# Performance work log

Hardware: AMD Instinct MI355X
Metric: run time of the kernel (lower is better)

Reference implementation:

```python
import jax, jax.numpy as jnp
import numpy as np

M = 8
EPS = 1e-5


def _bn(x, gamma, beta):
    # x: [T, N, C]; torch BatchNorm1d on [T, C, N] (training mode) normalizes
    # over batch and length dims -> axes (0, 1) here, biased variance.
    mean = jnp.mean(x, axis=(0, 1))
    var = jnp.var(x, axis=(0, 1))
    return (x - mean) * jax.lax.rsqrt(var + EPS) * gamma + beta


def setup_inputs() -> dict:
    key = jax.random.key(0)
    T, N, E = 128, 256, 128
    ks = jax.random.split(key, 16)
    s = 1.0 / np.sqrt(E)
    inp = {
        "node": jax.random.normal(ks[0], (T, N, E), dtype=jnp.float32),
        "Wq": jax.random.uniform(ks[1], (E, E), jnp.float32, -s, s),
        "bq": jax.random.uniform(ks[2], (E,), jnp.float32, -s, s),
        "Wk": jax.random.uniform(ks[3], (E, E), jnp.float32, -s, s),
        "bk": jax.random.uniform(ks[4], (E,), jnp.float32, -s, s),
        "Wv": jax.random.uniform(ks[5], (E, E), jnp.float32, -s, s),
        "bv": jax.random.uniform(ks[6], (E,), jnp.float32, -s, s),
        "Ww": jax.random.uniform(ks[7], (E, E), jnp.float32, -s, s),
        "bw": jax.random.uniform(ks[8], (E,), jnp.float32, -s, s),
        "Wf1": jax.random.uniform(ks[9], (4 * E, E), jnp.float32, -s, s),
        "bf1": jax.random.uniform(ks[10], (4 * E,), jnp.float32, -s, s),
        "Wf2": jax.random.uniform(ks[11], (E, 4 * E), jnp.float32, -0.5 * s, 0.5 * s),
        "bf2": jax.random.uniform(ks[12], (E,), jnp.float32, -0.5 * s, 0.5 * s),
        "g1": jnp.ones((E,), jnp.float32),
        "be1": jnp.zeros((E,), jnp.float32),
        "g2": jnp.ones((E,), jnp.float32),
        "be2": jnp.zeros((E,), jnp.float32),
        "temp_len": T,
    }
    return inp


def reference(node, Wq, bq, Wk, bk, Wv, bv, Ww, bw, Wf1, bf1, Wf2, bf2,
              g1, be1, g2, be2, temp_len):
    T, N, E = node.shape
    D = E // M          # head dim = 16
    dk = E / M          # softmax scale denominator (embedding_size / M)

    q = (node @ Wq.T + bq).reshape(T, N, M, D)
    k = (node @ Wk.T + bk).reshape(T, N, M, D)
    v = (node @ Wv.T + bv).reshape(T, N, M, D)

    # scores[t,n,j,m] = sum_d q[t,n,m,d]*k[t,j,m,d] / sqrt(dk)
    scores = jnp.einsum('tnmd,tjmd->tnjm', q, k) / jnp.sqrt(jnp.float32(dk))
    attn = jax.nn.softmax(scores, axis=2)  # softmax over key dim (dim=2)

    # out[t,n,m,d] = sum_j attn[t,n,j,m] * v[t,j,m,d]
    out = jnp.einsum('tnjm,tjmd->tnmd', attn, v).reshape(T, N, E)

    x = out @ Ww.T + bw + node
    x = _bn(x, g1, be1)

    x1 = jax.nn.relu(x @ Wf1.T + bf1) @ Wf2.T + bf2
    x = x + x1
    x = _bn(x, g2, be2)
    return x
```

## Files before the change

kernel.cpp:

```cpp
#include <hip/hip_runtime.h>
#include <stdint.h>

typedef unsigned int  uint32;
typedef unsigned short u16;
typedef __attribute__((ext_vector_type(8))) short short8;
typedef __attribute__((ext_vector_type(4))) float f32x4;
typedef __attribute__((ext_vector_type(4))) _Float16 half4;

__device__ __forceinline__ float bits2f(uint32 u){ union{uint32 u; float f;} c; c.u=u; return c.f; }
__device__ __forceinline__ uint32 f2bits(float f){ union{uint32 u; float f;} c; c.f=f; return c.u; }
__device__ __forceinline__ u16 f2b(float f){ uint32 u=f2bits(f); return (u16)((u + 0x7FFFu + ((u>>16)&1u))>>16); }
__device__ __forceinline__ float b2f(u16 h){ return bits2f(((uint32)h)<<16); }
__device__ __forceinline__ u16 f2h(float f){ _Float16 h=(_Float16)f; union{u16 u; _Float16 h;} c; c.h=h; return c.u; }
__device__ __forceinline__ float4 ld4f(const float* p){ return *(const float4*)p; }
#define BLO(u) bits2f((u)<<16)
#define BHI(u) bits2f((u)&0xFFFF0000u)

#define QKS 24

__device__ __forceinline__ void load_ab(const float* __restrict__ gacc,
                                        const float* __restrict__ gam,
                                        const float* __restrict__ bet,
                                        float* sA, float* sB, int t)
{
  if (t < 128) {
    const float mean = gacc[t] * (1.f/32768.f);
    const float var  = gacc[128 + t] * (1.f/32768.f) - mean * mean;
    const float rstd = rsqrtf(var + 1e-5f);
    const float Ac = gam[t] * rstd;
    sA[t] = Ac;
    sB[t] = bet[t] - mean * Ac;
  }
  __syncthreads();
}

template<int OMODE, int RES, bool RELU, bool AF32, bool WF32, bool BNA, bool STATS, int JT>
__device__ __forceinline__ void gemm_tile(
    u16* As, u16* Ws, const float* sA, const float* sB, float* pS, float* pQ,
    const void* Ain, const void* W, const float* bias, const void* res,
    float* gacc_out, void* out, int row0, int col0, int K, int Nout,
    float oscale, int t)
{
  constexpr int WROWS = JT * 32;
  const int L = t & 63, w = t >> 6;
  const int wrow = (w >> 1) * 64, wcol = (w & 1) * (JT * 16);
  const int lm = L & 15, lg = L >> 4;

  f32x4 acc[4][JT];
#pragma unroll
  for (int i = 0; i < 4; ++i)
#pragma unroll
    for (int j = 0; j < JT; ++j) acc[i][j] = (f32x4){0.f,0.f,0.f,0.f};

  const int srow = t >> 1, skc = (t & 1) * 32;
  const u16*   Ab = (const u16*)Ain + (size_t)(row0 + srow) * K + skc;
  const float* Af = (const float*)Ain + (size_t)(row0 + srow) * K + skc;
  u16* Asp = As + srow * 72 + skc;
  constexpr int TPR = 256 / WROWS;
  const int wsrow = t / TPR, wskc = (t % TPR) * (64 / TPR);
  const u16*   Wp  = (const u16*)W + (size_t)(col0 + wsrow) * K + wskc;
  const float* Wpf = (const float*)W + (size_t)(col0 + wsrow) * K + wskc;
  u16* Wsp = Ws + wsrow * 72 + wskc;
  constexpr int NW = (64 / TPR) / 8;

  for (int k0 = 0; k0 < K; k0 += 64) {
    short8 ga[4], gw[NW];
    if constexpr (AF32) {
#pragma unroll
      for (int i = 0; i < 4; ++i) {
        const float4 fa = ld4f(Af + k0 + i*8);
        const float4 fb = ld4f(Af + k0 + i*8 + 4);
        short8 s;
        s[0]=(short)f2b(fa.x); s[1]=(short)f2b(fa.y); s[2]=(short)f2b(fa.z); s[3]=(short)f2b(fa.w);
        s[4]=(short)f2b(fb.x); s[5]=(short)f2b(fb.y); s[6]=(short)f2b(fb.z); s[7]=(short)f2b(fb.w);
        ga[i] = s;
      }
    } else if constexpr (BNA) {
#pragma unroll
      for (int i = 0; i < 4; ++i) {
        const int c = skc + k0 + i*8;
        const short8 x8 = *(const short8*)(Ab + k0 + i*8);
        const float4 A0 = *(const float4*)&sA[c], A1 = *(const float4*)&sA[c+4];
        const float4 B0 = *(const float4*)&sB[c], B1 = *(const float4*)&sB[c+4];
        short8 s;
        s[0]=(short)f2b(b2f((u16)x8[0])*A0.x+B0.x); s[1]=(short)f2b(b2f((u16)x8[1])*A0.y+B0.y);
        s[2]=(short)f2b(b2f((u16)x8[2])*A0.z+B0.z); s[3]=(short)f2b(b2f((u16)x8[3])*A0.w+B0.w);
        s[4]=(short)f2b(b2f((u16)x8[4])*A1.x+B1.x); s[5]=(short)f2b(b2f((u16)x8[5])*A1.y+B1.y);
        s[6]=(short)f2b(b2f((u16)x8[6])*A1.z+B1.z); s[7]=(short)f2b(b2f((u16)x8[7])*A1.w+B1.w);
        ga[i] = s;
      }
    } else {
#pragma unroll
      for (int i = 0; i < 4; ++i) ga[i] = *(const short8*)(Ab + k0 + i*8);
    }
    if constexpr (WF32) {
#pragma unroll
      for (int i = 0; i < NW; ++i) {
        const float4 fa = ld4f(Wpf + k0 + i*8);
        const float4 fb = ld4f(Wpf + k0 + i*8 + 4);
        short8 s;
        s[0]=(short)f2b(fa.x); s[1]=(short)f2b(fa.y); s[2]=(short)f2b(fa.z); s[3]=(short)f2b(fa.w);
        s[4]=(short)f2b(fb.x); s[5]=(short)f2b(fb.y); s[6]=(short)f2b(fb.z); s[7]=(short)f2b(fb.w);
        gw[i] = s;
      }
    } else {
#pragma unroll
      for (int i = 0; i < NW; ++i) gw[i] = *(const short8*)(Wp + k0 + i*8);
    }
    __syncthreads();
#pragma unroll
    for (int i = 0; i < 4; ++i) *(short8*)(Asp + i*8) = ga[i];
#pragma unroll
    for (int i = 0; i < NW; ++i) *(short8*)(Wsp + i*8) = gw[i];
    __syncthreads();
#pragma unroll
    for (int ks = 0; ks < 64; ks += 32) {
      short8 af[4], wf[JT];
#pragma unroll
      for (int i = 0; i < 4; ++i)
        af[i] = *(const short8*)(As + (wrow + i*16 + lm) * 72 + ks + lg*8);
#pragma unroll
      for (int j = 0; j < JT; ++j)
        wf[j] = *(const short8*)(Ws + (wcol + j*16 + lm) * 72 + ks + lg*8);
#pragma unroll
      for (int i = 0; i < 4; ++i)
#pragma unroll
        for (int j = 0; j < JT; ++j)
          acc[i][j] = __builtin_amdgcn_mfma_f32_16x16x32_bf16(af[i], wf[j], acc[i][j], 0, 0, 0);
    }
  }

  float bj[JT];
#pragma unroll
  for (int j = 0; j < JT; ++j) bj[j] = bias[col0 + wcol + j*16 + lm];

  float stS[JT], stQ[JT];
#pragma unroll
  for (int j = 0; j < JT; ++j) { stS[j] = 0.f; stQ[j] = 0.f; }

#pragma unroll
  for (int i = 0; i < 4; ++i) {
    const int rowb = row0 + wrow + i*16 + lg*4;
#pragma unroll
    for (int j = 0; j < JT; ++j) {
      const int col = col0 + wcol + j*16 + lm;
      float ra = 0.f, rb = 0.f;
      if constexpr (RES == 3) { ra = sA[col & 127]; rb = sB[col & 127]; }
      if constexpr (OMODE == 3) {
        const int tt = rowb >> 8, n0 = rowb & 255;
        const int mh = col >> 4, d = col & 15;
        uint2 o;
        o.x = (uint32)f2h(acc[i][j][0] + bj[j]) | ((uint32)f2h(acc[i][j][1] + bj[j]) << 16);
        o.y = (uint32)f2h(acc[i][j][2] + bj[j]) | ((uint32)f2h(acc[i][j][3] + bj[j]) << 16);
        *(uint2*)((u16*)out + (((size_t)tt*8 + mh)*16 + d)*256 + n0) = o;
      } else {
#pragma unroll
        for (int r = 0; r < 4; ++r) {
          const int row = rowb + r;
          float v = acc[i][j][r] + bj[j];
          if constexpr (RES == 1) v += ((const float*)res)[(size_t)row*128 + col];
          if constexpr (RES == 3) v += b2f(((const u16*)res)[(size_t)row*128 + col]) * ra + rb;
          if constexpr (RELU) v = fmaxf(v, 0.f);
          if constexpr (STATS) { stS[j] += v; stQ[j] += v*v; }
          if constexpr (OMODE == 2) {
            const int tt = row >> 8, n = row & 255, mh = col >> 4, d = col & 15;
            ((u16*)out)[(((size_t)tt*8 + mh)*256 + n)*16 + d] = f2h(v * oscale);
          } else {
            ((u16*)out)[(size_t)row * Nout + col] = f2b(v);
          }
        }
      }
    }
  }

  if constexpr (STATS) {
    __syncthreads();
    if (t < 128) { pS[t] = 0.f; pQ[t] = 0.f; }
    __syncthreads();
#pragma unroll
    for (int j = 0; j < JT; ++j) {
      const int col = col0 + wcol + j*16 + lm;
      atomicAdd(&pS[col], stS[j]);
      atomicAdd(&pQ[col], stQ[j]);
    }
    __syncthreads();
    if (t < 128) {
      atomicAdd(&gacc_out[t],       pS[t]);
      atomicAdd(&gacc_out[128 + t], pQ[t]);
    }
  }
}

__global__ __launch_bounds__(256)
void qkv_k(const float* __restrict__ node,
           const float* __restrict__ Wq, const float* __restrict__ bq,
           const float* __restrict__ Wk, const float* __restrict__ bk,
           const float* __restrict__ Wv, const float* __restrict__ bv,
           const float* __restrict__ Ww, const float* __restrict__ Wf1,
           const float* __restrict__ Wf2,
           u16* __restrict__ qb, u16* __restrict__ kb, u16* __restrict__ vb,
           u16* __restrict__ wb, float* __restrict__ accbuf)
{
  const int bid = blockIdx.x, t = threadIdx.x;
  if (bid < 768) {
    __shared__ u16 As[128*72];
    __shared__ u16 Ws[128*72];
    __shared__ __align__(16) float sA[128], sB[128];
    __shared__ float pS[128], pQ[128];
    const int x = bid & 255, y = bid >> 8;
    const float QSCALE = 0.36067376022224085f;
    if (y == 0)
      gemm_tile<2,0,false,true,true,false,false,4>(As,Ws,sA,sB,pS,pQ, node, Wq, bq,
          nullptr, nullptr, qb, x*128, 0, 128, 128, QSCALE, t);
    else if (y == 1)
      gemm_tile<2,0,false,true,true,false,false,4>(As,Ws,sA,sB,pS,pQ, node, Wk, bk,
          nullptr, nullptr, kb, x*128, 0, 128, 128, 1.f, t);
    else
      gemm_tile<3,0,false,true,true,false,false,4>(As,Ws,sA,sB,pS,pQ, node, Wv, bv,
          nullptr, nullptr, vb, x*128, 0, 128, 128, 1.f, t);
  } else if (bid < 912) {
    const int i = (bid - 768) * 256 + t;
    const float4* src; u16* dst;
    if      (i <  4096) { src = (const float4*)Ww  + i;         dst = wb +  49152 + (size_t)i*4; }
    else if (i < 20480) { src = (const float4*)Wf1 + (i-4096);  dst = wb +  65536 + (size_t)(i-4096)*4; }
    else                { src = (const float4*)Wf2 + (i-20480); dst = wb + 131072 + (size_t)(i-20480)*4; }
    float4 v = *src;
    uint2 o;
    o.x = (uint32)f2b(v.x) | ((uint32)f2b(v.y) << 16);
    o.y = (uint32)f2b(v.z) | ((uint32)f2b(v.w) << 16);
    *(uint2*)dst = o;
  } else {
    accbuf[t] = 0.f;
    accbuf[256 + t] = 0.f;
  }
}

__global__ __launch_bounds__(256)
void oproj_k(const u16* __restrict__ ab, const u16* __restrict__ wwb,
             const float* __restrict__ bw, const float* __restrict__ node,
             float* __restrict__ accbuf, u16* __restrict__ xb)
{
  __shared__ u16 As[128*72];
  __shared__ u16 Ws[128*72];
  __shared__ __align__(16) float sA[128], sB[128];
  __shared__ float pS[128], pQ[128];
  gemm_tile<0,1,false,false,false,false,true,4>(As,Ws,sA,sB,pS,pQ, ab, wwb, bw,
      node, accbuf, xb, blockIdx.x*128, 0, 128, 128, 1.f, threadIdx.x);
}

__global__ __launch_bounds__(256)
void ffn1_k(const u16* __restrict__ xb, const u16* __restrict__ wf1b,
            const float* __restrict__ bf1, const float* __restrict__ accbuf,
            const float* __restrict__ g1, const float* __restrict__ be1,
            u16* __restrict__ hb)
{
  __shared__ u16 As[128*72];
  __shared__ u16 Ws[128*72];
  __shared__ __align__(16) float sA[128], sB[128];
  __shared__ float pS[128], pQ[128];
  load_ab(accbuf, g1, be1, sA, sB, threadIdx.x);
  gemm_tile<0,0,true,false,false,true,false,4>(As,Ws,sA,sB,pS,pQ, xb, wf1b, bf1,
      nullptr, nullptr, hb, blockIdx.x*128, blockIdx.y*128, 128, 512, 1.f, threadIdx.x);
}

__global__ __launch_bounds__(256)
void ffn2_k(const u16* __restrict__ hb, const u16* __restrict__ wf2b,
            const float* __restrict__ bf2, const u16* __restrict__ xb,
            const float* __restrict__ accbuf, const float* __restrict__ g1,
            const float* __restrict__ be1, float* __restrict__ acc2,
            u16* __restrict__ x2b)
{
  __shared__ u16 As[128*72];
  __shared__ u16 Ws[64*72];
  __shared__ __align__(16) float sA[128], sB[128];
  __shared__ float pS[128], pQ[128];
  load_ab(accbuf, g1, be1, sA, sB, threadIdx.x);
  gemm_tile<0,3,false,false,false,false,true,2>(As,Ws,sA,sB,pS,pQ, hb, wf2b, bf2,
      xb, acc2, x2b, blockIdx.x*128, blockIdx.y*64, 512, 128, 1.f, threadIdx.x);
}

__global__ __launch_bounds__(256)
void attn_k(const u16* __restrict__ q, const u16* __restrict__ k,
            const u16* __restrict__ v, u16* __restrict__ ab)
{
  __shared__ __align__(16) u16 Qs[256*QKS];
  __shared__ __align__(16) u16 Ks[256*QKS];
  __shared__ __align__(16) u16 Vt[16*264];
  const int tm = blockIdx.x, tt = tm >> 3, m = tm & 7;
  const int t = threadIdx.x;

  const uint4* qg = (const uint4*)(q + (size_t)tm*4096);
  const uint4* kg = (const uint4*)(k + (size_t)tm*4096);
  const uint4* vg = (const uint4*)(v + (size_t)tm*4096);
#pragma unroll
  for (int p = t; p < 512; p += 256) {
    const uint4 a = qg[p], b = kg[p], c = vg[p];
    const int row = p >> 1, h = (p & 1) * 8;
    *(uint4*)(Qs + row*QKS + h) = a;
    *(uint4*)(Ks + row*QKS + h) = b;
    *(uint4*)(Vt + (p >> 5)*264 + (p & 31)*8) = c;
  }
  __syncthreads();

  const int w = t >> 6, L = t & 63, lm = L & 15, quad = L >> 4;

  half4 vf[16];
#pragma unroll
  for (int jt = 0; jt < 16; ++jt)
    vf[jt] = *(const half4*)(Vt + lm*264 + jt*16 + quad*4);

  for (int nt = 0; nt < 4; ++nt) {
    const half4 bq = *(const half4*)(Qs + ((w*4 + nt)*16 + lm)*QKS + quad*4);
    f32x4 s[16];
#pragma unroll
    for (int jt = 0; jt < 16; ++jt) {
      const half4 af = *(const half4*)(Ks + (jt*16 + lm)*QKS + quad*4);
      s[jt] = __builtin_amdgcn_mfma_f32_16x16x16f16(af, bq, (f32x4){0.f,0.f,0.f,0.f}, 0, 0, 0);
    }
    float mx = s[0][0];
#pragma unroll
    for (int jt = 0; jt < 16; ++jt)
#pragma unroll
      for (int r = 0; r < 4; ++r) mx = fmaxf(mx, s[jt][r]);
    mx = fmaxf(mx, __shfl_xor(mx, 16));
    mx = fmaxf(mx, __shfl_xor(mx, 32));
    float ls = 0.f;
#pragma unroll
    for (int jt = 0; jt < 16; ++jt)
#pragma unroll
      for (int r = 0; r < 4; ++r) { const float p = exp2f(s[jt][r] - mx); s[jt][r] = p; ls += p; }
    ls += __shfl_xor(ls, 16);
    ls += __shfl_xor(ls, 32);

    f32x4 oacc = {0.f,0.f,0.f,0.f};
#pragma unroll
    for (int jt = 0; jt < 16; ++jt) {
      half4 pf;
      pf[0] = (_Float16)s[jt][0]; pf[1] = (_Float16)s[jt][1];
      pf[2] = (_Float16)s[jt][2]; pf[3] = (_Float16)s[jt][3];
      oacc = __builtin_amdgcn_mfma_f32_16x16x16f16(pf, vf[jt], oacc, 0, 0, 0);
    }
    const int q0 = w*64 + nt*16 + quad*4;
#pragma unroll
    for (int r = 0; r < 4; ++r) {
      const float lr = __shfl(ls, quad*4 + r);
      ab[((size_t)tt*256 + q0 + r)*128 + m*16 + lm] = f2b(oacc[r] / lr);
    }
  }
}

__global__ __launch_bounds__(256)
void bn_final(const uint32* __restrict__ x2, const float* __restrict__ gacc,
              const float* __restrict__ gam, const float* __restrict__ bet,
              float* __restrict__ out)
{
  __shared__ float sA[128], sB[128];
  const int t = threadIdx.x;
  load_ab(gacc, gam, bet, sA, sB, t);
#pragma unroll 4
  for (int kk = 0; kk < 16; ++kk) {
    const size_t idx = (size_t)blockIdx.x * 4096 + kk * 256 + t;
    const uint32 u = x2[idx];
    const int c = (int)((idx & 63) * 2);
    float2 o;
    o.x = BLO(u) * sA[c]   + sB[c];
    o.y = BHI(u) * sA[c+1] + sB[c+1];
    ((float2*)out)[idx] = o;
  }
}

extern "C" void kernel_launch(void* const* d_in, const int* in_sizes, int n_in,
                              void* d_out, int out_size, void* d_ws, size_t ws_size,
                              hipStream_t stream)
{
  (void)in_sizes; (void)n_in; (void)out_size; (void)ws_size;
  const float* node = (const float*)d_in[0];
  const float* Wq  = (const float*)d_in[1];  const float* bq  = (const float*)d_in[2];
  const float* Wk  = (const float*)d_in[3];  const float* bk  = (const float*)d_in[4];
  const float* Wv  = (const float*)d_in[5];  const float* bv  = (const float*)d_in[6];
  const float* Ww  = (const float*)d_in[7];  const float* bw  = (const float*)d_in[8];
  const float* Wf1 = (const float*)d_in[9];  const float* bf1 = (const float*)d_in[10];
  const float* Wf2 = (const float*)d_in[11]; const float* bf2 = (const float*)d_in[12];
  const float* g1  = (const float*)d_in[13]; const float* be1 = (const float*)d_in[14];
  const float* g2  = (const float*)d_in[15]; const float* be2 = (const float*)d_in[16];
  float* out = (float*)d_out;
  char* ws = (char*)d_ws;

  u16* wb  = (u16*)(ws + 0);
  u16* qb  = (u16*)(ws + 524288);
  u16* kb  = (u16*)(ws + 8912896);
  u16* vb  = (u16*)(ws + 17301504);
  u16* ab  = (u16*)(ws + 25690112);
  u16* xb  = (u16*)(ws + 34078720);
  u16* x2b = (u16*)(ws + 42467328);
  float* accbuf = (float*)(ws + 50855936);
  u16* hb  = qb;

  u16* wwb = wb + 49152;  u16* wf1b = wb + 65536; u16* wf2b = wb + 131072;

  dim3 blk(256);

  qkv_k<<<dim3(913), blk, 0, stream>>>(node, Wq,bq, Wk,bk, Wv,bv, Ww, Wf1, Wf2,
                                       qb, kb, vb, wb, accbuf);
  attn_k<<<dim3(1024), blk, 0, stream>>>(qb, kb, vb, ab);
  oproj_k<<<dim3(256), blk, 0, stream>>>(ab, wwb, bw, node, accbuf, xb);
  ffn1_k<<<dim3(256,4), blk, 0, stream>>>(xb, wf1b, bf1, accbuf, g1, be1, hb);
  ffn2_k<<<dim3(256,2), blk, 0, stream>>>(hb, wf2b, bf2, xb, accbuf, g1, be1,
                                          accbuf + 256, x2b);
  bn_final<<<dim3(512), blk, 0, stream>>>((const uint32*)x2b, accbuf + 256, g2, be2, out);
}
```

Baseline: 206.8 us.

## Prefetch next GEMM K-chunk into registers, split oproj columns, vectorize bn_final

The GEMM tile loop now issues global loads for the next 64-wide K chunk before the MFMA work on the current chunk, hiding load latency behind compute. Conversion to bf16 and the BN affine are moved to the shared-memory write step. The output projection is split into two 64-column blocks per row tile to double the grid size, and bn_final processes four values per thread with 16-byte stores. These add register pressure from the prefetch buffers, and the oproj column split must keep per-column statistics accumulation correct.

```diff
diff --git a/kernel.cpp b/kernel.cpp
--- a/kernel.cpp
+++ b/kernel.cpp
@@ -63,23 +63,48 @@
   u16* Wsp = Ws + wsrow * 72 + wskc;
   constexpr int NW = (64 / TPR) / 8;
 
-  for (int k0 = 0; k0 < K; k0 += 64) {
-    short8 ga[4], gw[NW];
+  short8 ga[4]; short8 gw[NW];
+  float4 fa[4][2]; float4 fw[NW][2];
+
+  auto load_chunk = [&](int k0) {
     if constexpr (AF32) {
 #pragma unroll
       for (int i = 0; i < 4; ++i) {
-        const float4 fa = ld4f(Af + k0 + i*8);
-        const float4 fb = ld4f(Af + k0 + i*8 + 4);
+        fa[i][0] = ld4f(Af + k0 + i*8);
+        fa[i][1] = ld4f(Af + k0 + i*8 + 4);
+      }
+    } else {
+#pragma unroll
+      for (int i = 0; i < 4; ++i) ga[i] = *(const short8*)(Ab + k0 + i*8);
+    }
+    if constexpr (WF32) {
+#pragma unroll
+      for (int i = 0; i < NW; ++i) {
+        fw[i][0] = ld4f(Wpf + k0 + i*8);
+        fw[i][1] = ld4f(Wpf + k0 + i*8 + 4);
+      }
+    } else {
+#pragma unroll
+      for (int i = 0; i < NW; ++i) gw[i] = *(const short8*)(Wp + k0 + i*8);
+    }
+  };
+
+  auto write_chunk = [&](int k0) {
+    if constexpr (AF32) {
+#pragma unroll
+      for (int i = 0; i < 4; ++i) {
         short8 s;
-        s[0]=(short)f2b(fa.x); s[1]=(short)f2b(fa.y); s[2]=(short)f2b(fa.z); s[3]=(short)f2b(fa.w);
-        s[4]=(short)f2b(fb.x); s[5]=(short)f2b(fb.y); s[6]=(short)f2b(fb.z); s[7]=(short)f2b(fb.w);
-        ga[i] = s;
+        s[0]=(short)f2b(fa[i][0].x); s[1]=(short)f2b(fa[i][0].y);
+        s[2]=(short)f2b(fa[i][0].z); s[3]=(short)f2b(fa[i][0].w);
+        s[4]=(short)f2b(fa[i][1].x); s[5]=(short)f2b(fa[i][1].y);
+        s[6]=(short)f2b(fa[i][1].z); s[7]=(short)f2b(fa[i][1].w);
+        *(short8*)(Asp + i*8) = s;
       }
     } else if constexpr (BNA) {
 #pragma unroll
       for (int i = 0; i < 4; ++i) {
         const int c = skc + k0 + i*8;
-        const short8 x8 = *(const short8*)(Ab + k0 + i*8);
+        const short8 x8 = ga[i];
         const float4 A0 = *(const float4*)&sA[c], A1 = *(const float4*)&sA[c+4];
         const float4 B0 = *(const float4*)&sB[c], B1 = *(const float4*)&sB[c+4];
         short8 s;
@@ -87,32 +112,34 @@
         s[2]=(short)f2b(b2f((u16)x8[2])*A0.z+B0.z); s[3]=(short)f2b(b2f((u16)x8[3])*A0.w+B0.w);
         s[4]=(short)f2b(b2f((u16)x8[4])*A1.x+B1.x); s[5]=(short)f2b(b2f((u16)x8[5])*A1.y+B1.y);
         s[6]=(short)f2b(b2f((u16)x8[6])*A1.z+B1.z); s[7]=(short)f2b(b2f((u16)x8[7])*A1.w+B1.w);
-        ga[i] = s;
+        *(short8*)(Asp + i*8) = s;
       }
     } else {
 #pragma unroll
-      for (int i = 0; i < 4; ++i) ga[i] = *(const short8*)(Ab + k0 + i*8);
+      for (int i = 0; i < 4; ++i) *(short8*)(Asp + i*8) = ga[i];
     }
     if constexpr (WF32) {
 #pragma unroll
       for (int i = 0; i < NW; ++i) {
-        const float4 fa = ld4f(Wpf + k0 + i*8);
-        const float4 fb = ld4f(Wpf + k0 + i*8 + 4);
         short8 s;
-        s[0]=(short)f2b(fa.x); s[1]=(short)f2b(fa.y); s[2]=(short)f2b(fa.z); s[3]=(short)f2b(fa.w);
-        s[4]=(short)f2b(fb.x); s[5]=(short)f2b(fb.y); s[6]=(short)f2b(fb.z); s[7]=(short)f2b(fb.w);
-        gw[i] = s;
+        s[0]=(short)f2b(fw[i][0].x); s[1]=(short)f2b(fw[i][0].y);
+        s[2]=(short)f2b(fw[i][0].z); s[3]=(short)f2b(fw[i][0].w);
+        s[4]=(short)f2b(fw[i][1].x); s[5]=(short)f2b(fw[i][1].y);
+        s[6]=(short)f2b(fw[i][1].z); s[7]=(short)f2b(fw[i][1].w);
+        *(short8*)(Wsp + i*8) = s;
       }
     } else {
 #pragma unroll
-      for (int i = 0; i < NW; ++i) gw[i] = *(const short8*)(Wp + k0 + i*8);
-    }
+      for (int i = 0; i < NW; ++i) *(short8*)(Wsp + i*8) = gw[i];
+    }
+  };
+
+  load_chunk(0);
+  for (int k0 = 0; k0 < K; k0 += 64) {
     __syncthreads();
-#pragma unroll
-    for (int i = 0; i < 4; ++i) *(short8*)(Asp + i*8) = ga[i];
-#pragma unroll
-    for (int i = 0; i < NW; ++i) *(short8*)(Wsp + i*8) = gw[i];
+    write_chunk(k0);
     __syncthreads();
+    if (k0 + 64 < K) load_chunk(k0 + 64);
 #pragma unroll
     for (int ks = 0; ks < 64; ks += 32) {
       short8 af[4], wf[JT];
@@ -241,11 +268,11 @@
              float* __restrict__ accbuf, u16* __restrict__ xb)
 {
   __shared__ u16 As[128*72];
-  __shared__ u16 Ws[128*72];
+  __shared__ u16 Ws[64*72];
   __shared__ __align__(16) float sA[128], sB[128];
   __shared__ float pS[128], pQ[128];
-  gemm_tile<0,1,false,false,false,false,true,4>(As,Ws,sA,sB,pS,pQ, ab, wwb, bw,
-      node, accbuf, xb, blockIdx.x*128, 0, 128, 128, 1.f, threadIdx.x);
+  gemm_tile<0,1,false,false,false,false,true,2>(As,Ws,sA,sB,pS,pQ, ab, wwb, bw,
+      node, accbuf, xb, blockIdx.x*128, blockIdx.y*64, 128, 128, 1.f, threadIdx.x);
 }
 
 __global__ __launch_bounds__(256)
@@ -350,22 +377,26 @@
 }
 
 __global__ __launch_bounds__(256)
-void bn_final(const uint32* __restrict__ x2, const float* __restrict__ gacc,
+void bn_final(const uint2* __restrict__ x2, const float* __restrict__ gacc,
               const float* __restrict__ gam, const float* __restrict__ bet,
               float* __restrict__ out)
 {
-  __shared__ float sA[128], sB[128];
+  __shared__ __align__(16) float sA[128], sB[128];
   const int t = threadIdx.x;
   load_ab(gacc, gam, bet, sA, sB, t);
-#pragma unroll 4
-  for (int kk = 0; kk < 16; ++kk) {
-    const size_t idx = (size_t)blockIdx.x * 4096 + kk * 256 + t;
-    const uint32 u = x2[idx];
-    const int c = (int)((idx & 63) * 2);
-    float2 o;
-    o.x = BLO(u) * sA[c]   + sB[c];
-    o.y = BHI(u) * sA[c+1] + sB[c+1];
-    ((float2*)out)[idx] = o;
+#pragma unroll 2
+  for (int kk = 0; kk < 8; ++kk) {
+    const size_t idx = (size_t)blockIdx.x * 2048 + kk * 256 + t;
+    const uint2 u = x2[idx];
+    const int c = (int)((idx & 31) * 4);
+    const f32x4 A = *(const f32x4*)&sA[c];
+    const f32x4 B = *(const f32x4*)&sB[c];
+    f32x4 o;
+    o[0] = BLO(u.x)*A[0] + B[0];
+    o[1] = BHI(u.x)*A[1] + B[1];
+    o[2] = BLO(u.y)*A[2] + B[2];
+    o[3] = BHI(u.y)*A[3] + B[3];
+    *(f32x4*)(out + idx*4) = o;
   }
 }
 
@@ -403,9 +434,9 @@
   qkv_k<<<dim3(913), blk, 0, stream>>>(node, Wq,bq, Wk,bk, Wv,bv, Ww, Wf1, Wf2,
                                        qb, kb, vb, wb, accbuf);
   attn_k<<<dim3(1024), blk, 0, stream>>>(qb, kb, vb, ab);
-  oproj_k<<<dim3(256), blk, 0, stream>>>(ab, wwb, bw, node, accbuf, xb);
+  oproj_k<<<dim3(256,2), blk, 0, stream>>>(ab, wwb, bw, node, accbuf, xb);
   ffn1_k<<<dim3(256,4), blk, 0, stream>>>(xb, wf1b, bf1, accbuf, g1, be1, hb);
   ffn2_k<<<dim3(256,2), blk, 0, stream>>>(hb, wf2b, bf2, xb, accbuf, g1, be1,
                                           accbuf + 256, x2b);
-  bn_final<<<dim3(512), blk, 0, stream>>>((const uint32*)x2b, accbuf + 256, g2, be2, out);
-}
+  bn_final<<<dim3(512), blk, 0, stream>>>((const uint2*)x2b, accbuf + 256, g2, be2, out);
+}
```

New measurement: 209.5 us. About the same (+1.3%).
